# Kernel optimization log

Measured on AMD Instinct MI355X. Metric: run time of the kernel, lower is better.

The kernel has to match this reference:

```python
import jax, jax.numpy as jnp
import numpy as np

HID = 512
HEADS = 8
PF = 2048
EPS = 1e-5


def _layernorm(x, g, b):
    mu = jnp.mean(x, axis=-1, keepdims=True)
    var = jnp.var(x, axis=-1, keepdims=True)
    return (x - mu) * jax.lax.rsqrt(var + EPS) * g + b


def setup_inputs() -> dict:
    key = jax.random.key(0)
    ks = jax.random.split(key, 20)
    s = 0.02
    inp = {
        "trg": jax.random.normal(ks[0], (16, 1024, HID), jnp.float32),
        "src": jax.random.normal(ks[1], (16, 1024, HID), jnp.float32),
        "ln_g": jnp.ones((HID,), jnp.float32),
        "ln_b": jnp.zeros((HID,), jnp.float32),
        "wq": jax.random.normal(ks[2], (HID, HID), jnp.float32) * s,
        "bq": jnp.zeros((HID,), jnp.float32),
        "wk": jax.random.normal(ks[3], (HID, HID), jnp.float32) * s,
        "bk": jnp.zeros((HID,), jnp.float32),
        "wv": jax.random.normal(ks[4], (HID, HID), jnp.float32) * s,
        "bv": jnp.zeros((HID,), jnp.float32),
        "wo": jax.random.normal(ks[5], (HID, HID), jnp.float32) * s,
        "bo": jnp.zeros((HID,), jnp.float32),
        "pf1_w": jax.random.normal(ks[6], (PF, HID), jnp.float32) * s,
        "pf1_b": jnp.zeros((PF,), jnp.float32),
        "pf2_w": jax.random.normal(ks[7], (HID, PF), jnp.float32) * s,
        "pf2_b": jnp.zeros((HID,), jnp.float32),
        "fc1_w": jax.random.normal(ks[8], (256, HID), jnp.float32) * s,
        "fc1_b": jnp.zeros((256,), jnp.float32),
        "fc2_w": jax.random.normal(ks[9], (2, 256), jnp.float32) * s,
        "fc2_b": jnp.zeros((2,), jnp.float32),
    }
    return inp


def reference(trg, src, ln_g, ln_b, wq, bq, wk, bk, wv, bv, wo, bo,
              pf1_w, pf1_b, pf2_w, pf2_b, fc1_w, fc1_b, fc2_w, fc2_b):
    B, T, D = trg.shape
    S = src.shape[1]
    dh = D // HEADS

    # --- multi-head attention (Q=trg, K=V=src, no mask; dropout=eval/no-op) ---
    q = (trg @ wq.T + bq).reshape(B, T, HEADS, dh)
    k = (src @ wk.T + bk).reshape(B, S, HEADS, dh)
    v = (src @ wv.T + bv).reshape(B, S, HEADS, dh)
    scores = jnp.einsum('bqhd,bkhd->bhqk', q, k) / jnp.sqrt(jnp.float32(dh))
    attn = jax.nn.softmax(scores, axis=-1)
    ctx = jnp.einsum('bhqk,bkhd->bqhd', attn, v).reshape(B, T, D)
    sa_out = ctx @ wo.T + bo

    x = _layernorm(trg + sa_out, ln_g, ln_b)

    # --- position-wise feed-forward ---
    h = jax.nn.relu(x @ pf1_w.T + pf1_b)
    ff = h @ pf2_w.T + pf2_b
    x = _layernorm(x + ff, ln_g, ln_b)

    # --- norm-weighted sum pooling over sequence (vectorized) ---
    norm = jnp.linalg.norm(x, axis=2)              # [B, T]
    w = jax.nn.softmax(norm, axis=1)               # [B, T]
    pooled = jnp.einsum('bt,btd->bd', w, x)        # [B, D]

    label = jax.nn.relu(pooled @ fc1_w.T + fc1_b) @ fc2_w.T + fc2_b
    return label
```

## Files before the change

kernel.cpp:

```cpp
#include <hip/hip_runtime.h>

typedef __bf16 bf16x8 __attribute__((ext_vector_type(8)));
typedef float f32x4 __attribute__((ext_vector_type(4)));
typedef unsigned short u16;

__device__ __forceinline__ u16 f2bf(float f){
  unsigned u = __builtin_bit_cast(unsigned, f);
  u += 0x7fffu + ((u>>16)&1u);
  return (u16)(u>>16);
}
__device__ __forceinline__ float bf2f(u16 h){
  unsigned u = ((unsigned)h)<<16; return __builtin_bit_cast(float,u);
}
__device__ __forceinline__ bf16x8 ld8(const u16* p){ return *(const bf16x8*)p; }
__device__ __forceinline__ f32x4 mfma16(bf16x8 a, bf16x8 b, f32x4 c){
  return __builtin_amdgcn_mfma_f32_16x16x32_bf16(a,b,c,0,0,0);
}
__device__ __forceinline__ void gl16(const u16* g, u16* l){
  __builtin_amdgcn_global_load_lds(
    (const __attribute__((address_space(1))) unsigned int*)g,
    (__attribute__((address_space(3))) unsigned int*)l, 16, 0, 0);
}
__device__ __forceinline__ unsigned cvtpk(float a, float b){
  unsigned r;
  asm("v_cvt_pk_bf16_f32 %0, %1, %2" : "=v"(r) : "v"(a), "v"(b));
  return r;
}

#define QSC 0.18033688f

__global__ __launch_bounds__(256) void k_split2(const float* __restrict__ a,
    const float* __restrict__ b, u16* __restrict__ da, u16* __restrict__ db, int n){
  const float* s = blockIdx.y ? b : a;
  u16* d = blockIdx.y ? db : da;
  int i = (blockIdx.x*256 + threadIdx.x)*4;
  const int stride = gridDim.x*256*4;
  for(; i<n; i+=stride){
    float4 v = *(const float4*)(s+i);
    ushort4 H = {f2bf(v.x),f2bf(v.y),f2bf(v.z),f2bf(v.w)};
    *(ushort4*)(d+i)=H;
  }
}

struct SplitW { const float* s[6]; u16* d[6]; int n[6]; };
__global__ __launch_bounds__(256) void k_splitw(SplitW P){
  const int y = blockIdx.y;
  const float* s = P.s[y]; u16* d = P.d[y]; const int n = P.n[y];
  int i = (blockIdx.x*256 + threadIdx.x)*4;
  const int stride = gridDim.x*256*4;
  for(; i<n; i+=stride){
    float4 v = *(const float4*)(s+i);
    ushort4 H = {f2bf(v.x),f2bf(v.y),f2bf(v.z),f2bf(v.w)};
    *(ushort4*)(d+i)=H;
  }
}

template<int EPI>
__global__ __launch_bounds__(256) void k_gemm(
  const u16* __restrict__ A, const u16* __restrict__ W,
  const float* __restrict__ bias, int M, int N, int K,
  float* __restrict__ Cf, u16* __restrict__ Oh)
{
  __shared__ __align__(16) u16 sA[2][128*32], sW[2][128*32];
  const int tid = threadIdx.x, w = tid>>6, l = tid&63;
  const int l15 = l&15, g = l>>4;
  const int gx = gridDim.x;
  const int bid = blockIdx.y*gx + blockIdx.x;
  const int nwg = gx*gridDim.y;
  const int wgid = (bid&7)*(nwg>>3) + (bid>>3);
  const int m0 = (wgid/gx)*128, n0 = (wgid%gx)*128;
  const int wr = (w>>1)*64, wc = (w&1)*64;
  f32x4 acc[4][4] = {};
  const int sr = l>>2, sslot = l&3;
  const int scol = 8*((sslot - (sr>>1)) & 3);
  int offA[4], offW[4];
  #pragma unroll
  for(int i=0;i<4;i++){ const int R = wr+i*16+l15; offA[i] = R*32 + ((g+(R>>1))&3)*8; }
  #pragma unroll
  for(int j=0;j<4;j++){ const int C = wc+j*16+l15; offW[j] = C*32 + ((g+(C>>1))&3)*8; }
  const u16* Ab = A + (long)m0*K + scol;
  const u16* Wb = W + (long)n0*K + scol;
  const int nk = K>>5;

#define G_STAGE(BUF, T) { \
    const int k0 = (T)<<5; \
    _Pragma("unroll") \
    for(int i=0;i<2;i++){ \
      const int rows = i*64 + w*16; \
      gl16(Ab + (long)(rows+sr)*K + k0, sA[BUF] + rows*32); \
      gl16(Wb + (long)(rows+sr)*K + k0, sW[BUF] + rows*32); \
    } }

#define G_STEP(CUR, T) { \
    if((T)+1 < nk) G_STAGE(CUR^1, (T)+1); \
    bf16x8 av[4], wv[4]; \
    _Pragma("unroll") for(int i=0;i<4;i++) av[i] = *(const bf16x8*)(sA[CUR]+offA[i]); \
    _Pragma("unroll") for(int j=0;j<4;j++) wv[j] = *(const bf16x8*)(sW[CUR]+offW[j]); \
    _Pragma("unroll") for(int j=0;j<4;j++){ \
      _Pragma("unroll") for(int i=0;i<4;i++) acc[i][j] = mfma16(av[i], wv[j], acc[i][j]); } \
    __syncthreads(); }

  G_STAGE(0,0); __syncthreads();
  for(int t=0;t<nk;t+=2){ G_STEP(0,t); G_STEP(1,t+1); }
#undef G_STAGE
#undef G_STEP

  #pragma unroll
  for(int i=0;i<4;i++){
    #pragma unroll
    for(int j=0;j<4;j++){
      const int col  = n0 + wc + j*16 + l15;
      const float bb = bias ? bias[col] : 0.f;
      const int rowb = m0 + wr + i*16 + g*4;
      #pragma unroll
      for(int jj=0;jj<4;jj++){
        float v = acc[i][j][jj] + bb;
        const int row = rowb + jj;
        if constexpr(EPI==0){ Cf[(long)row*N + col] = v; }
        else { Oh[(long)row*N + col] = f2bf(fmaxf(v,0.f)); }
      }
    }
  }
}

__global__ __launch_bounds__(256) void k_qkv(
  const u16* __restrict__ trg_hi, const u16* __restrict__ src_hi,
  const u16* __restrict__ Wh,
  const float* __restrict__ bq, const float* __restrict__ bk, const float* __restrict__ bv,
  u16* __restrict__ Qb, u16* __restrict__ Kb, u16* __restrict__ Vt)
{
  __shared__ __align__(16) u16 sA[2][128*32], sW[2][128*32];
  const int tid = threadIdx.x, w = tid>>6, l = tid&63;
  const int l15 = l&15, g = l>>4;
  const int bid = blockIdx.x;
  const int wgid = (bid&7)*192 + (bid>>3);
  const int m0 = (wgid/12)*128, n0 = (wgid%12)*128;
  const u16* A = (n0<512)? trg_hi : src_hi;
  const float* bp = (n0<512)? bq : (n0<1024? bk : bv);
  const int nb = (n0<512)? 0 : (n0<1024? 512 : 1024);
  const int wr = (w>>1)*64, wc = (w&1)*64;
  f32x4 acc[4][4] = {};
  const int sr = l>>2, sslot = l&3;
  const int scol = 8*((sslot - (sr>>1)) & 3);
  int offA[4], offW[4];
  #pragma unroll
  for(int i=0;i<4;i++){ const int R = wr+i*16+l15; offA[i] = R*32 + ((g+(R>>1))&3)*8; }
  #pragma unroll
  for(int j=0;j<4;j++){ const int C = wc+j*16+l15; offW[j] = C*32 + ((g+(C>>1))&3)*8; }
  const u16* Ab = A  + (long)m0*512 + scol;
  const u16* Wb = Wh + (long)n0*512 + scol;

#define Q_STAGE(BUF, T) { \
    const int k0 = (T)<<5; \
    _Pragma("unroll") \
    for(int i=0;i<2;i++){ \
      const int rows = i*64 + w*16; \
      gl16(Ab + (long)(rows+sr)*512 + k0, sA[BUF] + rows*32); \
      gl16(Wb + (long)(rows+sr)*512 + k0, sW[BUF] + rows*32); \
    } }

#define Q_STEP(CUR, T) { \
    if((T)+1 < 16) Q_STAGE(CUR^1, (T)+1); \
    bf16x8 av[4], wv[4]; \
    _Pragma("unroll") for(int i=0;i<4;i++) av[i] = *(const bf16x8*)(sA[CUR]+offA[i]); \
    _Pragma("unroll") for(int j=0;j<4;j++) wv[j] = *(const bf16x8*)(sW[CUR]+offW[j]); \
    _Pragma("unroll") for(int j=0;j<4;j++){ \
      _Pragma("unroll") for(int i=0;i<4;i++) acc[i][j] = mfma16(av[i], wv[j], acc[i][j]); } \
    __syncthreads(); }

  Q_STAGE(0,0); __syncthreads();
  for(int t=0;t<16;t+=2){ Q_STEP(0,t); Q_STEP(1,t+1); }
#undef Q_STAGE
#undef Q_STEP

  #pragma unroll
  for(int i=0;i<4;i++){
    #pragma unroll
    for(int j=0;j<4;j++){
      const int col = n0 + wc + j*16 + l15;
      const int cl  = col - nb;
      const float bb = bp[cl];
      const int rowb = m0 + wr + i*16 + g*4;
      #pragma unroll
      for(int jj=0;jj<4;jj++){
        float v = acc[i][j][jj] + bb;
        const int row = rowb + jj;
        if(n0 < 512){ Qb[(long)row*512 + cl] = f2bf(v*QSC); }
        else if(n0 < 1024){ Kb[(long)row*512 + cl] = f2bf(v); }
        else {
          const int h = cl>>6, d = cl&63;
          const long dst = (((long)(row>>10)*8 + h)*64 + d)*1024
                         + ((row>>6)&15)*64 + (row&15)*4 + ((row>>4)&3);
          Vt[dst] = f2bf(v);
        }
      }
    }
  }
}

__global__ __launch_bounds__(256) void k_attn(
  const u16* __restrict__ Q, const u16* __restrict__ K,
  const u16* __restrict__ Vt, u16* __restrict__ O)
{
  __shared__ __align__(16) u16 sK[2][64*64], sV[2][64*64];
  __shared__ __align__(16) u16 Ph[4][32*72];
  const int bid = blockIdx.x;
  const int wg = (bid&7)*128 + (bid>>3);
  const int q0 = (wg&7)*128, hd = (wg>>3)&7, b = wg>>6;
  const int tid = threadIdx.x, w = tid>>6, l = tid&63, l15 = l&15, g = l>>4;
  bf16x8 qf[2][2];
  #pragma unroll
  for(int rf=0;rf<2;rf++){
    const int qrow = q0 + rf*64 + w*16 + l15;
    const long qoff = (long)(b*1024 + qrow)*512 + hd*64 + g*8;
    qf[rf][0] = ld8(Q+qoff); qf[rf][1] = ld8(Q+qoff+32);
  }
  const int sr = l>>3, sslot = l&7;
  const int scol = 8*(sslot ^ (sr&7));
  const u16* Kb = K + (long)b*1024*512 + hd*64;
  const u16* Vb = Vt + (long)(b*8+hd)*64*1024;
  int offK[4][2], offV[2][4], offPw[2][4], offPr[2][2];
  #pragma unroll
  for(int sf=0;sf<4;sf++){
    const int row = sf*16 + l15;
    offK[sf][0] = row*64 + ((g    ^(row&7)))*8;
    offK[sf][1] = row*64 + (((g+4)^(row&7)))*8;
  }
  #pragma unroll
  for(int ss=0;ss<2;ss++){
    #pragma unroll
    for(int df=0;df<4;df++){
      const int row = df*16 + l15;
      offV[ss][df] = row*64 + (((ss*4+g)^(row&7)))*8;
    }
  }
  #pragma unroll
  for(int rf=0;rf<2;rf++){
    #pragma unroll
    for(int j=0;j<4;j++) offPw[rf][j] = (rf*16 + g*4 + j)*72 + l15*4;
    #pragma unroll
    for(int ss=0;ss<2;ss++) offPr[rf][ss] = (rf*16 + l15)*72 + ss*32 + g*8;
  }
  f32x4 rs[2] = {};
  f32x4 ctx[2][4] = {};

#define A_STAGE(BUF, T) { \
    const long soff = (long)(T)*64; \
    _Pragma("unroll") \
    for(int i=0;i<2;i++){ \
      const int rows = w*8 + i*32; \
      gl16(Kb + (soff+rows+sr)*512 + scol, sK[BUF] + rows*64); \
      gl16(Vb + (long)(rows+sr)*1024 + soff + scol, sV[BUF] + rows*64); \
    } }

#define A_TILE(CUR, T) { \
    if((T)+1 < 16) A_STAGE(CUR^1, (T)+1); \
    _Pragma("unroll") \
    for(int rf=0;rf<2;rf++){ \
      f32x4 sv[4]; \
      _Pragma("unroll") \
      for(int sf=0;sf<4;sf++){ \
        f32x4 a = {}; \
        a = mfma16(qf[rf][0], *(const bf16x8*)(sK[CUR]+offK[sf][0]), a); \
        a = mfma16(qf[rf][1], *(const bf16x8*)(sK[CUR]+offK[sf][1]), a); \
        sv[sf] = a; \
      } \
      float p[4][4]; \
      _Pragma("unroll") \
      for(int sf=0;sf<4;sf++){ \
        _Pragma("unroll") \
        for(int j=0;j<4;j++){ p[sf][j] = exp2f(sv[sf][j]); rs[rf][j] += p[sf][j]; } \
      } \
      _Pragma("unroll") \
      for(int j=0;j<4;j++){ \
        uint2 pk = { cvtpk(p[0][j], p[1][j]), cvtpk(p[2][j], p[3][j]) }; \
        *(uint2*)(&Ph[w][offPw[rf][j]]) = pk; \
      } \
    } \
    _Pragma("unroll") \
    for(int ss=0;ss<2;ss++){ \
      bf16x8 pa0 = *(const bf16x8*)(&Ph[w][offPr[0][ss]]); \
      bf16x8 pa1 = *(const bf16x8*)(&Ph[w][offPr[1][ss]]); \
      _Pragma("unroll") \
      for(int df=0;df<4;df++){ \
        const bf16x8 vf = *(const bf16x8*)(sV[CUR]+offV[ss][df]); \
        ctx[0][df] = mfma16(pa0, vf, ctx[0][df]); \
        ctx[1][df] = mfma16(pa1, vf, ctx[1][df]); \
      } \
    } \
    __syncthreads(); }

  A_STAGE(0,0); __syncthreads();
  for(int t=0;t<16;t+=2){ A_TILE(0,t); A_TILE(1,t+1); }
#undef A_STAGE
#undef A_TILE

  #pragma unroll
  for(int rf=0;rf<2;rf++){
    float inv[4];
    #pragma unroll
    for(int j=0;j<4;j++){
      float t = rs[rf][j];
      #pragma unroll
      for(int mask=1;mask<16;mask<<=1) t += __shfl_xor(t, mask);
      inv[j] = 1.f/t;
    }
    #pragma unroll
    for(int df=0;df<4;df++){
      #pragma unroll
      for(int j=0;j<4;j++){
        const float v = ctx[rf][df][j] * inv[j];
        const long off = (long)(b*1024 + q0 + rf*64 + w*16 + g*4 + j)*512 + hd*64 + df*16 + l15;
        O[off] = f2bf(v);
      }
    }
  }
}

__global__ __launch_bounds__(256) void k_ln(
  const float* __restrict__ xa, const float* __restrict__ xb,
  const float* __restrict__ gg, const float* __restrict__ bvec,
  float* __restrict__ yf, u16* __restrict__ yh,
  float* __restrict__ norms)
{
  const int w = threadIdx.x>>6, l = threadIdx.x&63;
  const long rrow = (long)blockIdx.x*4 + w;
  const long base = rrow*512 + l*8;
  float4 a0 = *(const float4*)(xa+base), a1 = *(const float4*)(xa+base+4);
  float4 b0 = *(const float4*)(xb+base), b1 = *(const float4*)(xb+base+4);
  float v[8] = {a0.x+b0.x, a0.y+b0.y, a0.z+b0.z, a0.w+b0.w,
                a1.x+b1.x, a1.y+b1.y, a1.z+b1.z, a1.w+b1.w};
  float s=0.f, q=0.f;
  #pragma unroll
  for(int j=0;j<8;j++){ s += v[j]; q += v[j]*v[j]; }
  #pragma unroll
  for(int mask=1;mask<64;mask<<=1){ s += __shfl_xor(s,mask); q += __shfl_xor(q,mask); }
  const float mu  = s*(1.f/512.f);
  const float var = q*(1.f/512.f) - mu*mu;
  const float rstd = rsqrtf(var + 1e-5f);
  float y[8]; float nq = 0.f;
  #pragma unroll
  for(int j=0;j<8;j++){
    const int c = l*8+j;
    y[j] = (v[j]-mu)*rstd*gg[c] + bvec[c];
    nq += y[j]*y[j];
  }
  float4 t0={y[0],y[1],y[2],y[3]}, t1={y[4],y[5],y[6],y[7]};
  *(float4*)(yf+base)=t0; *(float4*)(yf+base+4)=t1;
  if(yh){
    u16 hv[8];
    #pragma unroll
    for(int j=0;j<8;j++){ hv[j]=f2bf(y[j]); }
    ushort4 hh0={hv[0],hv[1],hv[2],hv[3]}, hh1={hv[4],hv[5],hv[6],hv[7]};
    *(ushort4*)(yh+base)=hh0; *(ushort4*)(yh+base+4)=hh1;
  }
  if(norms){
    #pragma unroll
    for(int mask=1;mask<64;mask<<=1) nq += __shfl_xor(nq,mask);
    if(l==0) norms[rrow] = sqrtf(nq);
  }
}

__global__ __launch_bounds__(256) void k_pool2(const float* __restrict__ x2,
   const float* __restrict__ norms, float* __restrict__ partial)
{
  const int b = blockIdx.y, tc = blockIdx.z;
  const int col = blockIdx.x*256 + threadIdx.x;
  __shared__ float wsm[1024];
  __shared__ float red[4];
  const int tid = threadIdx.x, w = tid>>6, l = tid&63;
  float lm = -1e30f;
  for(int i=tid;i<1024;i+=256){ const float n = norms[b*1024+i]; wsm[i]=n; lm=fmaxf(lm,n); }
  #pragma unroll
  for(int mask=1;mask<64;mask<<=1) lm = fmaxf(lm, __shfl_xor(lm,mask));
  __syncthreads();
  if(l==0) red[w]=lm;
  __syncthreads();
  const float bm = fmaxf(fmaxf(red[0],red[1]), fmaxf(red[2],red[3]));
  __syncthreads();
  float ls = 0.f;
  for(int i=tid;i<1024;i+=256){ const float e = __expf(wsm[i]-bm); wsm[i]=e; ls+=e; }
  #pragma unroll
  for(int mask=1;mask<64;mask<<=1) ls += __shfl_xor(ls,mask);
  __syncthreads();
  if(l==0) red[w]=ls;
  __syncthreads();
  const float inv = 1.f/(red[0]+red[1]+red[2]+red[3]);
  float acc = 0.f;
  const int t0 = tc*128;
  for(int t=t0;t<t0+128;t++) acc += wsm[t]*x2[((long)b*1024+t)*512 + col];
  partial[((long)tc*16 + b)*512 + col] = acc*inv;
}

__global__ __launch_bounds__(256) void k_poolr(const float* __restrict__ partial,
   float* __restrict__ pooled)
{
  const int i = blockIdx.x*256 + threadIdx.x;
  float a = 0.f;
  #pragma unroll
  for(int tc=0;tc<8;tc++) a += partial[tc*8192 + i];
  pooled[i] = a;
}

__global__ __launch_bounds__(256) void k_head(const float* __restrict__ pooled,
  const float* __restrict__ w1, const float* __restrict__ b1,
  const float* __restrict__ w2, const float* __restrict__ b2,
  float* __restrict__ out)
{
  __shared__ float ps[16*512];
  __shared__ float h1[16*256];
  const int tid = threadIdx.x;
  for(int i=tid;i<16*512;i+=256) ps[i]=pooled[i];
  __syncthreads();
  float acc[16] = {};
  for(int k=0;k<512;k++){
    const float wv = w1[tid*512+k];
    #pragma unroll
    for(int i=0;i<16;i++) acc[i] += ps[i*512+k]*wv;
  }
  #pragma unroll
  for(int i=0;i<16;i++) h1[i*256+tid] = fmaxf(acc[i]+b1[tid], 0.f);
  __syncthreads();
  if(tid<32){
    const int i = tid>>1, o = tid&1;
    float a = b2[o];
    for(int k=0;k<256;k++) a += h1[i*256+k]*w2[o*256+k];
    out[i*2+o] = a;
  }
}

extern "C" void kernel_launch(void* const* d_in, const int* in_sizes, int n_in,
                              void* d_out, int out_size, void* d_ws, size_t ws_size,
                              hipStream_t stream)
{
  const float* trg  = (const float*)d_in[0];
  const float* src  = (const float*)d_in[1];
  const float* ln_g = (const float*)d_in[2];
  const float* ln_b = (const float*)d_in[3];
  const float* wq   = (const float*)d_in[4];  const float* bq  = (const float*)d_in[5];
  const float* wk   = (const float*)d_in[6];  const float* bk  = (const float*)d_in[7];
  const float* wv   = (const float*)d_in[8];  const float* bv  = (const float*)d_in[9];
  const float* wo   = (const float*)d_in[10]; const float* bo  = (const float*)d_in[11];
  const float* pf1w = (const float*)d_in[12]; const float* pf1b= (const float*)d_in[13];
  const float* pf2w = (const float*)d_in[14]; const float* pf2b= (const float*)d_in[15];
  const float* fc1w = (const float*)d_in[16]; const float* fc1b= (const float*)d_in[17];
  const float* fc2w = (const float*)d_in[18]; const float* fc2b= (const float*)d_in[19];
  float* out = (float*)d_out;

  char* ws = (char*)d_ws;
  const size_t PL = (size_t)16384*512*2;
  auto P = [&](int i)->u16*{ return (u16*)(ws + (size_t)i*PL); };
  u16 *src_hi=P(0), *trg_hi=P(1);
  u16 *Qb=P(2), *Kb=P(3), *Vt=P(4), *ctx=P(5);
  float* sa  = (float*)(ws + 0*PL);
  float* x1f = (float*)(ws + 2*PL);
  u16 *x1_hi = P(4);
  u16 *h_hi  = P(5);
  float* ffb = (float*)(ws + 0*PL);
  float* x2  = (float*)(ws + 5*PL);
  size_t off = 9*PL;
  auto carve = [&](size_t n)->char*{ char* p = ws+off; off += n; return p; };
  u16* wqkv_hi=(u16*)carve((size_t)1536*512*2);
  u16* wo_hi=(u16*)carve(512*512*2);
  u16* p1_hi=(u16*)carve((size_t)2048*512*2);
  u16* p2_hi=(u16*)carve((size_t)512*2048*2);
  float* norms  = (float*)carve(16384*4);
  float* partial= (float*)carve(8*16*512*4);
  float* pooled = (float*)carve(16*512*4);
  (void)ws_size; (void)in_sizes; (void)n_in; (void)out_size;

  const int NTOK = 16384;

  k_split2<<<dim3(8192,2),256,0,stream>>>(trg, src, trg_hi, src_hi, NTOK*512);
  SplitW sw;
  sw.s[0]=wq;  sw.d[0]=wqkv_hi;           sw.n[0]=512*512;
  sw.s[1]=wk;  sw.d[1]=wqkv_hi+512*512;   sw.n[1]=512*512;
  sw.s[2]=wv;  sw.d[2]=wqkv_hi+1024*512;  sw.n[2]=512*512;
  sw.s[3]=wo;  sw.d[3]=wo_hi;             sw.n[3]=512*512;
  sw.s[4]=pf1w; sw.d[4]=p1_hi;            sw.n[4]=2048*512;
  sw.s[5]=pf2w; sw.d[5]=p2_hi;            sw.n[5]=512*2048;
  k_splitw<<<dim3(512,6),256,0,stream>>>(sw);

  k_qkv<<<dim3(1536),256,0,stream>>>(trg_hi,src_hi,wqkv_hi,bq,bk,bv,Qb,Kb,Vt);

  k_attn<<<dim3(1024),256,0,stream>>>(Qb,Kb,Vt,ctx);

  k_gemm<0><<<dim3(4,128),256,0,stream>>>(ctx,wo_hi,bo,NTOK,512,512,sa,nullptr);
  k_ln<<<dim3(4096),256,0,stream>>>(trg, sa, ln_g, ln_b, x1f, x1_hi, nullptr);

  k_gemm<2><<<dim3(16,128),256,0,stream>>>(x1_hi,p1_hi,pf1b,NTOK,2048,512,nullptr,h_hi);
  k_gemm<0><<<dim3(4,128),256,0,stream>>>(h_hi,p2_hi,pf2b,NTOK,512,2048,ffb,nullptr);
  k_ln<<<dim3(4096),256,0,stream>>>(x1f, ffb, ln_g, ln_b, x2, nullptr, norms);

  k_pool2<<<dim3(2,16,8),256,0,stream>>>(x2, norms, partial);
  k_poolr<<<dim3(32),256,0,stream>>>(partial, pooled);
  k_head<<<1,256,0,stream>>>(pooled, fc1w, fc1b, fc2w, fc2b, out);
}
```

Before: 349.0 us.

## Restructure attention kernel to 8 waves with one query tile each, single-buffered

```diff
diff --git a/kernel.cpp b/kernel.cpp
--- a/kernel.cpp
+++ b/kernel.cpp
@@ -198,121 +198,83 @@
   }
 }
 
-__global__ __launch_bounds__(256) void k_attn(
+__global__ __launch_bounds__(512) void k_attn(
   const u16* __restrict__ Q, const u16* __restrict__ K,
   const u16* __restrict__ Vt, u16* __restrict__ O)
 {
-  __shared__ __align__(16) u16 sK[2][64*64], sV[2][64*64];
-  __shared__ __align__(16) u16 Ph[4][32*72];
+  __shared__ __align__(16) u16 sK[64*64], sV[64*64];
+  __shared__ __align__(16) u16 Ph[8][16*72];
   const int bid = blockIdx.x;
   const int wg = (bid&7)*128 + (bid>>3);
   const int q0 = (wg&7)*128, hd = (wg>>3)&7, b = wg>>6;
   const int tid = threadIdx.x, w = tid>>6, l = tid&63, l15 = l&15, g = l>>4;
-  bf16x8 qf[2][2];
-  #pragma unroll
-  for(int rf=0;rf<2;rf++){
-    const int qrow = q0 + rf*64 + w*16 + l15;
-    const long qoff = (long)(b*1024 + qrow)*512 + hd*64 + g*8;
-    qf[rf][0] = ld8(Q+qoff); qf[rf][1] = ld8(Q+qoff+32);
-  }
-  const int sr = l>>3, sslot = l&7;
-  const int scol = 8*(sslot ^ (sr&7));
+  const int qrow = q0 + w*16 + l15;
+  const long qoff = (long)(b*1024 + qrow)*512 + hd*64 + g*8;
+  bf16x8 qf[2] = { ld8(Q+qoff), ld8(Q+qoff+32) };
+  const int srw = l>>3, sslot = l&7;
+  const int scol = 8*(sslot ^ srw);
+  const int rows = w*8;
   const u16* Kb = K + (long)b*1024*512 + hd*64;
   const u16* Vb = Vt + (long)(b*8+hd)*64*1024;
-  int offK[4][2], offV[2][4], offPw[2][4], offPr[2][2];
-  #pragma unroll
-  for(int sf=0;sf<4;sf++){
-    const int row = sf*16 + l15;
-    offK[sf][0] = row*64 + ((g    ^(row&7)))*8;
-    offK[sf][1] = row*64 + (((g+4)^(row&7)))*8;
-  }
-  #pragma unroll
-  for(int ss=0;ss<2;ss++){
-    #pragma unroll
-    for(int df=0;df<4;df++){
-      const int row = df*16 + l15;
-      offV[ss][df] = row*64 + (((ss*4+g)^(row&7)))*8;
-    }
-  }
-  #pragma unroll
-  for(int rf=0;rf<2;rf++){
-    #pragma unroll
-    for(int j=0;j<4;j++) offPw[rf][j] = (rf*16 + g*4 + j)*72 + l15*4;
-    #pragma unroll
-    for(int ss=0;ss<2;ss++) offPr[rf][ss] = (rf*16 + l15)*72 + ss*32 + g*8;
-  }
-  f32x4 rs[2] = {};
-  f32x4 ctx[2][4] = {};
-
-#define A_STAGE(BUF, T) { \
-    const long soff = (long)(T)*64; \
-    _Pragma("unroll") \
-    for(int i=0;i<2;i++){ \
-      const int rows = w*8 + i*32; \
-      gl16(Kb + (soff+rows+sr)*512 + scol, sK[BUF] + rows*64); \
-      gl16(Vb + (long)(rows+sr)*1024 + soff + scol, sV[BUF] + rows*64); \
-    } }
-
-#define A_TILE(CUR, T) { \
-    if((T)+1 < 16) A_STAGE(CUR^1, (T)+1); \
-    _Pragma("unroll") \
-    for(int rf=0;rf<2;rf++){ \
-      f32x4 sv[4]; \
-      _Pragma("unroll") \
-      for(int sf=0;sf<4;sf++){ \
-        f32x4 a = {}; \
-        a = mfma16(qf[rf][0], *(const bf16x8*)(sK[CUR]+offK[sf][0]), a); \
-        a = mfma16(qf[rf][1], *(const bf16x8*)(sK[CUR]+offK[sf][1]), a); \
-        sv[sf] = a; \
-      } \
-      float p[4][4]; \
-      _Pragma("unroll") \
-      for(int sf=0;sf<4;sf++){ \
-        _Pragma("unroll") \
-        for(int j=0;j<4;j++){ p[sf][j] = exp2f(sv[sf][j]); rs[rf][j] += p[sf][j]; } \
-      } \
-      _Pragma("unroll") \
-      for(int j=0;j<4;j++){ \
-        uint2 pk = { cvtpk(p[0][j], p[1][j]), cvtpk(p[2][j], p[3][j]) }; \
-        *(uint2*)(&Ph[w][offPw[rf][j]]) = pk; \
-      } \
-    } \
-    _Pragma("unroll") \
-    for(int ss=0;ss<2;ss++){ \
-      bf16x8 pa0 = *(const bf16x8*)(&Ph[w][offPr[0][ss]]); \
-      bf16x8 pa1 = *(const bf16x8*)(&Ph[w][offPr[1][ss]]); \
-      _Pragma("unroll") \
-      for(int df=0;df<4;df++){ \
-        const bf16x8 vf = *(const bf16x8*)(sV[CUR]+offV[ss][df]); \
-        ctx[0][df] = mfma16(pa0, vf, ctx[0][df]); \
-        ctx[1][df] = mfma16(pa1, vf, ctx[1][df]); \
-      } \
-    } \
-    __syncthreads(); }
-
-  A_STAGE(0,0); __syncthreads();
-  for(int t=0;t<16;t+=2){ A_TILE(0,t); A_TILE(1,t+1); }
-#undef A_STAGE
-#undef A_TILE
-
-  #pragma unroll
-  for(int rf=0;rf<2;rf++){
-    float inv[4];
-    #pragma unroll
-    for(int j=0;j<4;j++){
-      float t = rs[rf][j];
+  f32x4 rs = {};
+  f32x4 ctx[4] = {};
+  for(int s0=0;s0<1024;s0+=64){
+    gl16(Kb + (long)(s0+rows+srw)*512 + scol, sK + rows*64);
+    gl16(Vb + (long)(rows+srw)*1024 + s0 + scol, sV + rows*64);
+    __syncthreads();
+    f32x4 sv[4];
+    #pragma unroll
+    for(int sf=0;sf<4;sf++){
+      const int row = sf*16 + l15;
+      f32x4 a = {};
       #pragma unroll
-      for(int mask=1;mask<16;mask<<=1) t += __shfl_xor(t, mask);
-      inv[j] = 1.f/t;
-    }
-    #pragma unroll
-    for(int df=0;df<4;df++){
+      for(int h=0;h<2;h++){
+        const int ch = (g + 4*h) ^ (row&7);
+        a = mfma16(qf[h], *(const bf16x8*)(sK + row*64 + ch*8), a);
+      }
+      sv[sf] = a;
+    }
+    float p[4][4];
+    #pragma unroll
+    for(int sf=0;sf<4;sf++){
       #pragma unroll
       for(int j=0;j<4;j++){
-        const float v = ctx[rf][df][j] * inv[j];
-        const long off = (long)(b*1024 + q0 + rf*64 + w*16 + g*4 + j)*512 + hd*64 + df*16 + l15;
-        O[off] = f2bf(v);
+        p[sf][j] = exp2f(sv[sf][j]);
+        rs[j] += p[sf][j];
       }
+    }
+    #pragma unroll
+    for(int j=0;j<4;j++){
+      uint2 pk = { cvtpk(p[0][j], p[1][j]), cvtpk(p[2][j], p[3][j]) };
+      *(uint2*)(&Ph[w][(g*4+j)*72 + l15*4]) = pk;
+    }
+    #pragma unroll
+    for(int ss=0;ss<2;ss++){
+      bf16x8 pa = *(const bf16x8*)(&Ph[w][l15*72 + ss*32 + g*8]);
+      #pragma unroll
+      for(int df=0;df<4;df++){
+        const int row = df*16 + l15;
+        const int ch = (ss*4 + g) ^ (row&7);
+        ctx[df] = mfma16(pa, *(const bf16x8*)(sV + row*64 + ch*8), ctx[df]);
+      }
+    }
+    __syncthreads();
+  }
+  float inv[4];
+  #pragma unroll
+  for(int j=0;j<4;j++){
+    float t = rs[j];
+    #pragma unroll
+    for(int mask=1;mask<16;mask<<=1) t += __shfl_xor(t, mask);
+    inv[j] = 1.f/t;
+  }
+  #pragma unroll
+  for(int df=0;df<4;df++){
+    #pragma unroll
+    for(int j=0;j<4;j++){
+      const float v = ctx[df][j] * inv[j];
+      const long off = (long)(b*1024 + q0 + w*16 + g*4 + j)*512 + hd*64 + df*16 + l15;
+      O[off] = f2bf(v);
     }
   }
 }
@@ -483,7 +445,7 @@
 
   k_qkv<<<dim3(1536),256,0,stream>>>(trg_hi,src_hi,wqkv_hi,bq,bk,bv,Qb,Kb,Vt);
 
-  k_attn<<<dim3(1024),256,0,stream>>>(Qb,Kb,Vt,ctx);
+  k_attn<<<dim3(1024),512,0,stream>>>(Qb,Kb,Vt,ctx);
 
   k_gemm<0><<<dim3(4,128),256,0,stream>>>(ctx,wo_hi,bo,NTOK,512,512,sa,nullptr);
   k_ln<<<dim3(4096),256,0,stream>>>(trg, sa, ln_g, ln_b, x1f, x1_hi, nullptr);
```

Measured after the change: 340.3 us. -2.5%, faster.
